# Kernel optimization log

Measured on AMD Instinct MI355X. Metric: run time of the kernel, lower is better.

## Reference

```python
import jax, jax.numpy as jnp
import numpy as np

B, S, D = 8, 1024, 768
H, HD = 12, 64  # heads, head dim (H*HD == D)
EPS = 1e-12


def setup_inputs() -> dict:
    key = jax.random.key(0)
    ks = jax.random.split(key, 8)
    s = 0.02
    return {
        "hidden_states": jax.random.normal(ks[0], (B, S, D), jnp.float32),
        "attention_mask": jnp.zeros((B, 1, 1, S), jnp.float32),
        "head_mask": jnp.ones((H,), jnp.float32),
        "Wq": jax.random.normal(ks[1], (D, H * HD), jnp.float32) * s,
        "bq": jnp.zeros((H * HD,), jnp.float32),
        "Wk": jax.random.normal(ks[2], (D, H * HD), jnp.float32) * s,
        "bk": jnp.zeros((H * HD,), jnp.float32),
        "Wv": jax.random.normal(ks[3], (D, H * HD), jnp.float32) * s,
        "bv": jnp.zeros((H * HD,), jnp.float32),
        "Wo": jax.random.normal(ks[4], (D, H * HD), jnp.float32) * s,  # torch Linear weight [out=D, in=H*HD]
        "bo": jnp.zeros((D,), jnp.float32),
        "gamma": jnp.ones((D,), jnp.float32),
        "beta": jnp.zeros((D,), jnp.float32),
    }


def reference(hidden_states, attention_mask, head_mask, Wq, bq, Wk, bk, Wv, bv, Wo, bo, gamma, beta):
    def heads(x):  # [B,S,H*HD] -> [B,H,S,HD]
        return x.reshape(B, S, H, HD).transpose(0, 2, 1, 3)

    q = heads(hidden_states @ Wq.T + bq)
    k = heads(hidden_states @ Wk.T + bk)
    v = heads(hidden_states @ Wv.T + bv)

    scores = jnp.einsum("bhqd,bhkd->bhqk", q, k) / np.sqrt(HD).astype(np.float32)
    scores = scores + attention_mask
    probs = jax.nn.softmax(scores, axis=-1)  # dropout p=0 (eval)
    ctx = jnp.einsum("bhqk,bhkd->bhqd", probs, v)  # [B,H,S,HD]

    # masked per-head output projection: Wo.T.view(H, HD, D)
    Wph = Wo.T.reshape(H, HD, D)
    proj = jnp.einsum("bhsd,hde,h->bse", ctx, Wph, head_mask) + bo

    # residual + LayerNorm
    x = proj + hidden_states
    mu = jnp.mean(x, axis=-1, keepdims=True)
    var = jnp.mean(jnp.square(x - mu), axis=-1, keepdims=True)
    out = (x - mu) * jax.lax.rsqrt(var + EPS) * gamma + beta
    return out
```

## Files before the change

### kernel.cpp

```cpp
#include <hip/hip_runtime.h>
#include <hip/hip_bf16.h>
#include <math.h>

#define Bn 8
#define Sn 1024
#define Dn 768
#define Hn 12
#define MROWS (Bn * Sn)

typedef __attribute__((ext_vector_type(8))) short short8;
typedef __attribute__((ext_vector_type(4))) float floatx4;

__device__ __forceinline__ unsigned short f2b(float x) {
    union { float f; unsigned u; } v; v.f = x;
    unsigned r = v.u + 0x7fffu + ((v.u >> 16) & 1u);
    return (unsigned short)(r >> 16);
}

__device__ __forceinline__ void gload16(const void* g, void* l) {
    __builtin_amdgcn_global_load_lds(
        (const __attribute__((address_space(1))) void*)g,
        (__attribute__((address_space(3))) void*)l, 16, 0, 0);
}

__global__ __launch_bounds__(256) void convert_all(const float* __restrict__ X,
                                                   const float* __restrict__ Wq, const float* __restrict__ Wk,
                                                   const float* __restrict__ Wv, const float* __restrict__ Wo,
                                                   unsigned short* __restrict__ Xb,
                                                   unsigned short* __restrict__ Wqb, unsigned short* __restrict__ Wkb,
                                                   unsigned short* __restrict__ Wvb, unsigned short* __restrict__ Wob) {
    const int id = blockIdx.x;
    const float* src;
    unsigned short* dst;
    int i;
    if (id < 6144) {
        src = X; dst = Xb;
        i = id * 256 + threadIdx.x;
    } else {
        const int y = (id - 6144) / 576;
        src = (y == 0) ? Wq : (y == 1) ? Wk : (y == 2) ? Wv : Wo;
        dst = (y == 0) ? Wqb : (y == 1) ? Wkb : (y == 2) ? Wvb : Wob;
        i = ((id - 6144) % 576) * 256 + threadIdx.x;
    }
    float4 v = reinterpret_cast<const float4*>(src)[i];
    ushort4 o;
    o.x = f2b(v.x); o.y = f2b(v.y); o.z = f2b(v.z); o.w = f2b(v.w);
    reinterpret_cast<ushort4*>(dst)[i] = o;
}

__global__ __launch_bounds__(256) void gemm_qkv(const unsigned short* __restrict__ A,
                                                const unsigned short* __restrict__ Wq,
                                                const unsigned short* __restrict__ Wk,
                                                const unsigned short* __restrict__ Wv,
                                                const float* __restrict__ bq,
                                                const float* __restrict__ bk,
                                                const float* __restrict__ bv,
                                                unsigned short* __restrict__ Qh,
                                                unsigned short* __restrict__ Kh,
                                                unsigned short* __restrict__ Vt) {
    __shared__ __align__(16) unsigned short As[128 * 64];
    __shared__ __align__(16) unsigned short Ws[128 * 64];
    const int id = blockIdx.x;
    const int by = id & 63;
    const int bx = id >> 6;
    const int mat = bx / 6;
    const int m0 = by * 128;
    const int n0 = (bx % 6) * 128;
    const unsigned short* W = (mat == 0) ? Wq : (mat == 1) ? Wk : Wv;
    const float* bias = (mat == 0) ? bq : (mat == 1) ? bk : bv;
    unsigned short* Cout = (mat == 0) ? Qh : (mat == 1) ? Kh : Vt;

    const int tid = threadIdx.x;
    const int w = tid >> 6, l = tid & 63, quad = l >> 4, mr = l & 15;
    const int wm = (w >> 1) * 64, wn = (w & 1) * 64;

    const unsigned short* gAsrc[4];
    const unsigned short* gWsrc[4];
    unsigned short* lAdst[4];
    unsigned short* lWdst[4];
#pragma unroll
    for (int j = 0; j < 4; j++) {
        const int u = tid + j * 256;
        const int r = u >> 3, c = u & 7;
        const int kq = (c ^ (r & 7)) * 8;
        gAsrc[j] = &A[(size_t)(m0 + r) * Dn + kq];
        gWsrc[j] = &W[(size_t)(n0 + r) * Dn + kq];
        lAdst[j] = &As[u * 8];
        lWdst[j] = &Ws[u * 8];
    }

    int aoff[4][2], woff[4][2];
#pragma unroll
    for (int i = 0; i < 4; i++) {
        const int ra = wm + i * 16 + mr;
        const int rw = wn + i * 16 + mr;
#pragma unroll
        for (int ks = 0; ks < 2; ks++) {
            aoff[i][ks] = (ra * 8 + ((quad + ks * 4) ^ (ra & 7))) * 8;
            woff[i][ks] = (rw * 8 + ((quad + ks * 4) ^ (rw & 7))) * 8;
        }
    }

    floatx4 acc[4][4];
#pragma unroll
    for (int i = 0; i < 4; i++)
#pragma unroll
        for (int j = 0; j < 4; j++) {
            floatx4 z = {0.f, 0.f, 0.f, 0.f};
            acc[i][j] = z;
        }

    for (int kt = 0; kt < 12; kt++) {
        const int k0 = kt * 64;
        __syncthreads();
#pragma unroll
        for (int j = 0; j < 4; j++) {
            gload16(gAsrc[j] + k0, lAdst[j]);
            gload16(gWsrc[j] + k0, lWdst[j]);
        }
        __syncthreads();

        short8 af[4][2], bf[4][2];
#pragma unroll
        for (int i = 0; i < 4; i++)
#pragma unroll
            for (int ks = 0; ks < 2; ks++) {
                af[i][ks] = *(const short8*)&As[aoff[i][ks]];
                bf[i][ks] = *(const short8*)&Ws[woff[i][ks]];
            }
#pragma unroll
        for (int ks = 0; ks < 2; ks++)
#pragma unroll
            for (int i = 0; i < 4; i++)
#pragma unroll
                for (int j = 0; j < 4; j++)
                    acc[i][j] = __builtin_amdgcn_mfma_f32_16x16x32_bf16(af[i][ks], bf[j][ks], acc[i][j], 0, 0, 0);
    }

#pragma unroll
    for (int j = 0; j < 4; j++) {
        const int col = n0 + wn + j * 16 + mr;
        const float bval = bias[col];
        const int h = col >> 6, d = col & 63;
#pragma unroll
        for (int i = 0; i < 4; i++) {
#pragma unroll
            for (int r = 0; r < 4; r++) {
                const int m = m0 + wm + i * 16 + quad * 4 + r;
                const float val = acc[i][j][r] + bval;
                const int b = m >> 10, s = m & 1023;
                const size_t base = (size_t)(b * Hn + h) << 16;
                if (mat == 2)
                    Cout[base + (size_t)d * 1024 + s] = f2b(val);
                else
                    Cout[base + (size_t)s * 64 + d] = f2b(val);
            }
        }
    }
}

__global__ __launch_bounds__(256) void gemm_out(const unsigned short* __restrict__ A,
                                                const unsigned short* __restrict__ W,
                                                const float* __restrict__ bias,
                                                const float* __restrict__ X,
                                                float* __restrict__ xres) {
    __shared__ __align__(16) unsigned short As[64 * 64];
    __shared__ __align__(16) unsigned short Ws[128 * 64];
    const int id = blockIdx.x;
    const int by = id & 127;
    const int bx = id >> 7;
    const int m0 = by * 64;
    const int n0 = bx * 128;

    const int tid = threadIdx.x;
    const int w = tid >> 6, l = tid & 63, quad = l >> 4, mr = l & 15;

    const unsigned short* gAsrc[2];
    unsigned short* lAdst[2];
#pragma unroll
    for (int j = 0; j < 2; j++) {
        const int u = tid + j * 256;
        const int r = u >> 3, c = u & 7;
        gAsrc[j] = &A[(size_t)(m0 + r) * Dn + (c ^ (r & 7)) * 8];
        lAdst[j] = &As[u * 8];
    }
    const unsigned short* gWsrc[4];
    unsigned short* lWdst[4];
#pragma unroll
    for (int j = 0; j < 4; j++) {
        const int u = tid + j * 256;
        const int r = u >> 3, c = u & 7;
        gWsrc[j] = &W[(size_t)(n0 + r) * Dn + (c ^ (r & 7)) * 8];
        lWdst[j] = &Ws[u * 8];
    }

    int aoff[4][2], woff[2][2];
#pragma unroll
    for (int i = 0; i < 4; i++) {
        const int ra = i * 16 + mr;
#pragma unroll
        for (int ks = 0; ks < 2; ks++)
            aoff[i][ks] = (ra * 8 + ((quad + ks * 4) ^ (ra & 7))) * 8;
    }
#pragma unroll
    for (int j = 0; j < 2; j++) {
        const int rw = w * 32 + j * 16 + mr;
#pragma unroll
        for (int ks = 0; ks < 2; ks++)
            woff[j][ks] = (rw * 8 + ((quad + ks * 4) ^ (rw & 7))) * 8;
    }

    floatx4 acc[4][2];
#pragma unroll
    for (int i = 0; i < 4; i++)
#pragma unroll
        for (int j = 0; j < 2; j++) {
            floatx4 z = {0.f, 0.f, 0.f, 0.f};
            acc[i][j] = z;
        }

    for (int kt = 0; kt < 12; kt++) {
        const int k0 = kt * 64;
        __syncthreads();
#pragma unroll
        for (int j = 0; j < 2; j++) gload16(gAsrc[j] + k0, lAdst[j]);
#pragma unroll
        for (int j = 0; j < 4; j++) gload16(gWsrc[j] + k0, lWdst[j]);
        __syncthreads();

        short8 af[4][2], bf[2][2];
#pragma unroll
        for (int i = 0; i < 4; i++)
#pragma unroll
            for (int ks = 0; ks < 2; ks++)
                af[i][ks] = *(const short8*)&As[aoff[i][ks]];
#pragma unroll
        for (int j = 0; j < 2; j++)
#pragma unroll
            for (int ks = 0; ks < 2; ks++)
                bf[j][ks] = *(const short8*)&Ws[woff[j][ks]];
#pragma unroll
        for (int ks = 0; ks < 2; ks++)
#pragma unroll
            for (int i = 0; i < 4; i++)
#pragma unroll
                for (int j = 0; j < 2; j++)
                    acc[i][j] = __builtin_amdgcn_mfma_f32_16x16x32_bf16(af[i][ks], bf[j][ks], acc[i][j], 0, 0, 0);
    }

#pragma unroll
    for (int j = 0; j < 2; j++) {
        const int col = n0 + w * 32 + j * 16 + mr;
        const float bval = bias[col];
#pragma unroll
        for (int i = 0; i < 4; i++) {
#pragma unroll
            for (int r = 0; r < 4; r++) {
                const int m = m0 + i * 16 + quad * 4 + r;
                xres[(size_t)m * Dn + col] = acc[i][j][r] + bval + X[(size_t)m * Dn + col];
            }
        }
    }
}

__global__ __launch_bounds__(256) void flash_attn_mfma(const unsigned short* __restrict__ Qh,
                                                       const unsigned short* __restrict__ Kh,
                                                       const unsigned short* __restrict__ Vt,
                                                       const float* __restrict__ mask,
                                                       const float* __restrict__ head_mask,
                                                       unsigned short* __restrict__ ctx) {
    __shared__ __align__(16) unsigned short Ks[64 * 72];
    __shared__ __align__(16) unsigned short Vs[64 * 72];
    __shared__ __align__(16) unsigned short Ps[128 * 72];
    __shared__ float msk[64];

    const int id = blockIdx.x;
    const int bh = id % 96;
    const int qt = id / 96;
    const int b = bh / Hn, h = bh % Hn;
    const int q0 = qt * 128;
    const int tid = threadIdx.x;
    const int w = tid >> 6, l = tid & 63, quad = l >> 4, mr = l & 15;
    const size_t hb = (size_t)(b * Hn + h) << 16;

    short8 aq[2][2];
#pragma unroll
    for (int i = 0; i < 2; i++)
#pragma unroll
        for (int ks = 0; ks < 2; ks++)
            aq[i][ks] = *(const short8*)&Qh[hb + (size_t)(q0 + w * 32 + i * 16 + mr) * 64 + ks * 32 + quad * 8];

    float l_s[2][4];
    floatx4 oacc[2][4];
#pragma unroll
    for (int i = 0; i < 2; i++) {
#pragma unroll
        for (int r = 0; r < 4; r++) l_s[i][r] = 0.f;
#pragma unroll
        for (int jj = 0; jj < 4; jj++) {
            floatx4 z = {0.f, 0.f, 0.f, 0.f};
            oacc[i][jj] = z;
        }
    }

    const int srow = tid >> 2;
    const int scol = (tid & 3) * 16;

    short8 pk0 = *(const short8*)&Kh[hb + (size_t)srow * 64 + scol];
    short8 pk1 = *(const short8*)&Kh[hb + (size_t)srow * 64 + scol + 8];
    short8 pv0 = *(const short8*)&Vt[hb + (size_t)srow * 1024 + scol];
    short8 pv1 = *(const short8*)&Vt[hb + (size_t)srow * 1024 + scol + 8];
    float pm = mask[b * Sn + (tid & 63)];

    for (int kt = 0; kt < Sn / 64; kt++) {
        __syncthreads();
        *(short8*)&Ks[srow * 72 + scol] = pk0;
        *(short8*)&Ks[srow * 72 + scol + 8] = pk1;
        *(short8*)&Vs[srow * 72 + scol] = pv0;
        *(short8*)&Vs[srow * 72 + scol + 8] = pv1;
        if (tid < 64) msk[tid] = pm;
        if (kt < Sn / 64 - 1) {
            const int k0 = (kt + 1) * 64;
            pk0 = *(const short8*)&Kh[hb + (size_t)(k0 + srow) * 64 + scol];
            pk1 = *(const short8*)&Kh[hb + (size_t)(k0 + srow) * 64 + scol + 8];
            pv0 = *(const short8*)&Vt[hb + (size_t)srow * 1024 + k0 + scol];
            pv1 = *(const short8*)&Vt[hb + (size_t)srow * 1024 + k0 + scol + 8];
            pm = mask[b * Sn + k0 + (tid & 63)];
        }
        __syncthreads();

        floatx4 sacc[2][4];
#pragma unroll
        for (int i = 0; i < 2; i++)
#pragma unroll
            for (int j = 0; j < 4; j++) {
                floatx4 z = {0.f, 0.f, 0.f, 0.f};
                sacc[i][j] = z;
            }
#pragma unroll
        for (int ks = 0; ks < 2; ks++) {
#pragma unroll
            for (int j = 0; j < 4; j++) {
                short8 bk = *(const short8*)&Ks[(j * 16 + mr) * 72 + ks * 32 + quad * 8];
                sacc[0][j] = __builtin_amdgcn_mfma_f32_16x16x32_bf16(aq[0][ks], bk, sacc[0][j], 0, 0, 0);
                sacc[1][j] = __builtin_amdgcn_mfma_f32_16x16x32_bf16(aq[1][ks], bk, sacc[1][j], 0, 0, 0);
            }
        }

#pragma unroll
        for (int i = 0; i < 2; i++) {
#pragma unroll
            for (int j = 0; j < 4; j++) {
                const float mk = msk[j * 16 + mr];
#pragma unroll
                for (int r = 0; r < 4; r++) {
                    const float p = __expf(sacc[i][j][r] * 0.125f + mk);
                    l_s[i][r] += p;
                    Ps[(w * 32 + i * 16 + quad * 4 + r) * 72 + j * 16 + mr] = f2b(p);
                }
            }
        }

#pragma unroll
        for (int ks = 0; ks < 2; ks++) {
            short8 ap0 = *(const short8*)&Ps[(w * 32 + mr) * 72 + ks * 32 + quad * 8];
            short8 ap1 = *(const short8*)&Ps[(w * 32 + 16 + mr) * 72 + ks * 32 + quad * 8];
#pragma unroll
            for (int jj = 0; jj < 4; jj++) {
                short8 bv = *(const short8*)&Vs[(jj * 16 + mr) * 72 + ks * 32 + quad * 8];
                oacc[0][jj] = __builtin_amdgcn_mfma_f32_16x16x32_bf16(ap0, bv, oacc[0][jj], 0, 0, 0);
                oacc[1][jj] = __builtin_amdgcn_mfma_f32_16x16x32_bf16(ap1, bv, oacc[1][jj], 0, 0, 0);
            }
        }
    }

    const float hm = head_mask[h];
    float inv[2][4];
#pragma unroll
    for (int i = 0; i < 2; i++)
#pragma unroll
        for (int r = 0; r < 4; r++) {
            float t = l_s[i][r];
            t += __shfl_xor(t, 1);
            t += __shfl_xor(t, 2);
            t += __shfl_xor(t, 4);
            t += __shfl_xor(t, 8);
            inv[i][r] = hm / t;
        }
#pragma unroll
    for (int i = 0; i < 2; i++)
#pragma unroll
        for (int jj = 0; jj < 4; jj++)
#pragma unroll
            for (int r = 0; r < 4; r++) {
                const int qrow = q0 + w * 32 + i * 16 + quad * 4 + r;
                ctx[(size_t)(b * Sn + qrow) * Dn + h * 64 + jj * 16 + mr] = f2b(oacc[i][jj][r] * inv[i][r]);
            }
}

__global__ __launch_bounds__(256) void ln_kernel(const float* __restrict__ x,
                                                 const float* __restrict__ gamma,
                                                 const float* __restrict__ beta,
                                                 float* __restrict__ out) {
    __shared__ float r1[4];
    __shared__ float r2[4];
    const int m = blockIdx.x;
    const int tid = threadIdx.x;
    const int w = tid >> 6, lane = tid & 63;

    float xv[3];
    float s = 0.f, ss = 0.f;
#pragma unroll
    for (int i = 0; i < 3; i++) {
        int j = tid + i * 256;
        float t = x[(size_t)m * Dn + j];
        xv[i] = t;
        s += t;
        ss += t * t;
    }
#pragma unroll
    for (int o = 1; o < 64; o <<= 1) {
        s += __shfl_xor(s, o);
        ss += __shfl_xor(ss, o);
    }
    if (lane == 0) { r1[w] = s; r2[w] = ss; }
    __syncthreads();
    const float sum = r1[0] + r1[1] + r1[2] + r1[3];
    const float sqs = r2[0] + r2[1] + r2[2] + r2[3];
    const float mu = sum * (1.0f / Dn);
    const float var = sqs * (1.0f / Dn) - mu * mu;
    const float rstd = rsqrtf(var + 1e-12f);
#pragma unroll
    for (int i = 0; i < 3; i++) {
        int j = tid + i * 256;
        out[(size_t)m * Dn + j] = (xv[i] - mu) * rstd * gamma[j] + beta[j];
    }
}

extern "C" void kernel_launch(void* const* d_in, const int* in_sizes, int n_in,
                              void* d_out, int out_size, void* d_ws, size_t ws_size,
                              hipStream_t stream) {
    const float* X         = (const float*)d_in[0];
    const float* mask      = (const float*)d_in[1];
    const float* head_mask = (const float*)d_in[2];
    const float* Wq        = (const float*)d_in[3];
    const float* bq        = (const float*)d_in[4];
    const float* Wk        = (const float*)d_in[5];
    const float* bk        = (const float*)d_in[6];
    const float* Wv        = (const float*)d_in[7];
    const float* bv        = (const float*)d_in[8];
    const float* Wo        = (const float*)d_in[9];
    const float* bo        = (const float*)d_in[10];
    const float* gamma     = (const float*)d_in[11];
    const float* beta      = (const float*)d_in[12];
    float* out = (float*)d_out;

    const size_t NE = (size_t)Bn * Sn * Dn;
    const size_t NW = (size_t)Dn * Dn;

    char* p = (char*)d_ws;
    unsigned short* Xb  = (unsigned short*)p;  p += NE * 2;
    unsigned short* Wqb = (unsigned short*)p;  p += NW * 2;
    unsigned short* Wkb = (unsigned short*)p;  p += NW * 2;
    unsigned short* Wvb = (unsigned short*)p;  p += NW * 2;
    unsigned short* Wob = (unsigned short*)p;  p += NW * 2;
    unsigned short* Qh  = (unsigned short*)p;  p += NE * 2;
    unsigned short* Kh  = (unsigned short*)p;  p += NE * 2;
    unsigned short* Vtb = (unsigned short*)p;  p += NE * 2;
    unsigned short* ctx = (unsigned short*)p;  p += NE * 2;
    float* xres = (float*)p;

    convert_all<<<8448, 256, 0, stream>>>(X, Wq, Wk, Wv, Wo, Xb, Wqb, Wkb, Wvb, Wob);

    gemm_qkv<<<1152, 256, 0, stream>>>(Xb, Wqb, Wkb, Wvb, bq, bk, bv, Qh, Kh, Vtb);

    flash_attn_mfma<<<768, 256, 0, stream>>>(Qh, Kh, Vtb, mask, head_mask, ctx);

    gemm_out<<<768, 256, 0, stream>>>(ctx, Wob, bo, X, xres);

    ln_kernel<<<MROWS, 256, 0, stream>>>(xres, gamma, beta, out);
}
```

Baseline: 224.9 us.

## Double-buffer LDS tiles in QKV and output GEMMs, vectorize V-transpose stores

Both projection GEMMs now keep two LDS buffers, so the next K-tile's global-to-LDS loads are issued before computing on the current tile. This hides global load latency and halves the barriers per K step. The QKV epilogue also writes the transposed V output as packed 4-element stores instead of scalar ones. The cost is doubled LDS use per block, which may lower occupancy.

```diff
diff --git a/kernel.cpp b/kernel.cpp
--- a/kernel.cpp
+++ b/kernel.cpp
@@ -48,6 +48,21 @@
     reinterpret_cast<ushort4*>(dst)[i] = o;
 }
 
+#define QKV_COMPUTE(Ab, Wb)                                                    \
+    {                                                                          \
+        short8 af[4][2], bf[4][2];                                             \
+        _Pragma("unroll") for (int i = 0; i < 4; i++)                          \
+            _Pragma("unroll") for (int ks = 0; ks < 2; ks++) {                 \
+                af[i][ks] = *(const short8*)&(Ab)[aoff[i][ks]];                \
+                bf[i][ks] = *(const short8*)&(Wb)[woff[i][ks]];                \
+            }                                                                  \
+        _Pragma("unroll") for (int ks = 0; ks < 2; ks++)                       \
+            _Pragma("unroll") for (int i = 0; i < 4; i++)                      \
+                _Pragma("unroll") for (int j = 0; j < 4; j++)                  \
+                    acc[i][j] = __builtin_amdgcn_mfma_f32_16x16x32_bf16(       \
+                        af[i][ks], bf[j][ks], acc[i][j], 0, 0, 0);             \
+    }
+
 __global__ __launch_bounds__(256) void gemm_qkv(const unsigned short* __restrict__ A,
                                                 const unsigned short* __restrict__ Wq,
                                                 const unsigned short* __restrict__ Wk,
@@ -58,8 +73,8 @@
                                                 unsigned short* __restrict__ Qh,
                                                 unsigned short* __restrict__ Kh,
                                                 unsigned short* __restrict__ Vt) {
-    __shared__ __align__(16) unsigned short As[128 * 64];
-    __shared__ __align__(16) unsigned short Ws[128 * 64];
+    __shared__ __align__(16) unsigned short As[2][128 * 64];
+    __shared__ __align__(16) unsigned short Ws[2][128 * 64];
     const int id = blockIdx.x;
     const int by = id & 63;
     const int bx = id >> 6;
@@ -85,8 +100,8 @@
         const int kq = (c ^ (r & 7)) * 8;
         gAsrc[j] = &A[(size_t)(m0 + r) * Dn + kq];
         gWsrc[j] = &W[(size_t)(n0 + r) * Dn + kq];
-        lAdst[j] = &As[u * 8];
-        lWdst[j] = &Ws[u * 8];
+        lAdst[j] = &As[0][u * 8];
+        lWdst[j] = &Ws[0][u * 8];
     }
 
     int aoff[4][2], woff[4][2];
@@ -110,31 +125,38 @@
             acc[i][j] = z;
         }
 
-    for (int kt = 0; kt < 12; kt++) {
-        const int k0 = kt * 64;
+    const unsigned short* Af = &As[0][0];
+    const unsigned short* Wf = &Ws[0][0];
+
+#pragma unroll
+    for (int j = 0; j < 4; j++) {
+        gload16(gAsrc[j], lAdst[j]);
+        gload16(gWsrc[j], lWdst[j]);
+    }
+    __syncthreads();
+
+    for (int kt = 0; kt < 12; kt += 2) {
+        {
+            const int k0 = (kt + 1) * 64;
+#pragma unroll
+            for (int j = 0; j < 4; j++) {
+                gload16(gAsrc[j] + k0, lAdst[j] + 8192);
+                gload16(gWsrc[j] + k0, lWdst[j] + 8192);
+            }
+        }
+        QKV_COMPUTE(Af, Wf);
         __syncthreads();
-#pragma unroll
-        for (int j = 0; j < 4; j++) {
-            gload16(gAsrc[j] + k0, lAdst[j]);
-            gload16(gWsrc[j] + k0, lWdst[j]);
-        }
+
+        if (kt + 2 < 12) {
+            const int k0 = (kt + 2) * 64;
+#pragma unroll
+            for (int j = 0; j < 4; j++) {
+                gload16(gAsrc[j] + k0, lAdst[j]);
+                gload16(gWsrc[j] + k0, lWdst[j]);
+            }
+        }
+        QKV_COMPUTE(Af + 8192, Wf + 8192);
         __syncthreads();
-
-        short8 af[4][2], bf[4][2];
-#pragma unroll
-        for (int i = 0; i < 4; i++)
-#pragma unroll
-            for (int ks = 0; ks < 2; ks++) {
-                af[i][ks] = *(const short8*)&As[aoff[i][ks]];
-                bf[i][ks] = *(const short8*)&Ws[woff[i][ks]];
-            }
-#pragma unroll
-        for (int ks = 0; ks < 2; ks++)
-#pragma unroll
-            for (int i = 0; i < 4; i++)
-#pragma unroll
-                for (int j = 0; j < 4; j++)
-                    acc[i][j] = __builtin_amdgcn_mfma_f32_16x16x32_bf16(af[i][ks], bf[j][ks], acc[i][j], 0, 0, 0);
     }
 
 #pragma unroll
@@ -144,28 +166,50 @@
         const int h = col >> 6, d = col & 63;
 #pragma unroll
         for (int i = 0; i < 4; i++) {
-#pragma unroll
-            for (int r = 0; r < 4; r++) {
-                const int m = m0 + wm + i * 16 + quad * 4 + r;
-                const float val = acc[i][j][r] + bval;
-                const int b = m >> 10, s = m & 1023;
-                const size_t base = (size_t)(b * Hn + h) << 16;
-                if (mat == 2)
-                    Cout[base + (size_t)d * 1024 + s] = f2b(val);
-                else
-                    Cout[base + (size_t)s * 64 + d] = f2b(val);
-            }
-        }
-    }
-}
+            const int mbase = m0 + wm + i * 16 + quad * 4;
+            const int b = mbase >> 10, s0 = mbase & 1023;
+            const size_t base = (size_t)(b * Hn + h) << 16;
+            if (mat == 2) {
+                ushort4 o;
+                o.x = f2b(acc[i][j][0] + bval);
+                o.y = f2b(acc[i][j][1] + bval);
+                o.z = f2b(acc[i][j][2] + bval);
+                o.w = f2b(acc[i][j][3] + bval);
+                *reinterpret_cast<ushort4*>(&Cout[base + (size_t)d * 1024 + s0]) = o;
+            } else {
+#pragma unroll
+                for (int r = 0; r < 4; r++) {
+                    const float val = acc[i][j][r] + bval;
+                    Cout[base + (size_t)(s0 + r) * 64 + d] = f2b(val);
+                }
+            }
+        }
+    }
+}
+
+#define OUT_COMPUTE(Ab, Wb)                                                    \
+    {                                                                          \
+        short8 af[4][2], bf[2][2];                                             \
+        _Pragma("unroll") for (int i = 0; i < 4; i++)                          \
+            _Pragma("unroll") for (int ks = 0; ks < 2; ks++)                   \
+                af[i][ks] = *(const short8*)&(Ab)[aoff[i][ks]];                \
+        _Pragma("unroll") for (int j = 0; j < 2; j++)                          \
+            _Pragma("unroll") for (int ks = 0; ks < 2; ks++)                   \
+                bf[j][ks] = *(const short8*)&(Wb)[woff[j][ks]];                \
+        _Pragma("unroll") for (int ks = 0; ks < 2; ks++)                       \
+            _Pragma("unroll") for (int i = 0; i < 4; i++)                      \
+                _Pragma("unroll") for (int j = 0; j < 2; j++)                  \
+                    acc[i][j] = __builtin_amdgcn_mfma_f32_16x16x32_bf16(       \
+                        af[i][ks], bf[j][ks], acc[i][j], 0, 0, 0);             \
+    }
 
 __global__ __launch_bounds__(256) void gemm_out(const unsigned short* __restrict__ A,
                                                 const unsigned short* __restrict__ W,
                                                 const float* __restrict__ bias,
                                                 const float* __restrict__ X,
                                                 float* __restrict__ xres) {
-    __shared__ __align__(16) unsigned short As[64 * 64];
-    __shared__ __align__(16) unsigned short Ws[128 * 64];
+    __shared__ __align__(16) unsigned short As[2][64 * 64];
+    __shared__ __align__(16) unsigned short Ws[2][128 * 64];
     const int id = blockIdx.x;
     const int by = id & 127;
     const int bx = id >> 7;
@@ -182,7 +226,7 @@
         const int u = tid + j * 256;
         const int r = u >> 3, c = u & 7;
         gAsrc[j] = &A[(size_t)(m0 + r) * Dn + (c ^ (r & 7)) * 8];
-        lAdst[j] = &As[u * 8];
+        lAdst[j] = &As[0][u * 8];
     }
     const unsigned short* gWsrc[4];
     unsigned short* lWdst[4];
@@ -191,7 +235,7 @@
         const int u = tid + j * 256;
         const int r = u >> 3, c = u & 7;
         gWsrc[j] = &W[(size_t)(n0 + r) * Dn + (c ^ (r & 7)) * 8];
-        lWdst[j] = &Ws[u * 8];
+        lWdst[j] = &Ws[0][u * 8];
     }
 
     int aoff[4][2], woff[2][2];
@@ -219,33 +263,35 @@
             acc[i][j] = z;
         }
 
-    for (int kt = 0; kt < 12; kt++) {
-        const int k0 = kt * 64;
+    const unsigned short* Af = &As[0][0];
+    const unsigned short* Wf = &Ws[0][0];
+
+#pragma unroll
+    for (int j = 0; j < 2; j++) gload16(gAsrc[j], lAdst[j]);
+#pragma unroll
+    for (int j = 0; j < 4; j++) gload16(gWsrc[j], lWdst[j]);
+    __syncthreads();
+
+    for (int kt = 0; kt < 12; kt += 2) {
+        {
+            const int k0 = (kt + 1) * 64;
+#pragma unroll
+            for (int j = 0; j < 2; j++) gload16(gAsrc[j] + k0, lAdst[j] + 4096);
+#pragma unroll
+            for (int j = 0; j < 4; j++) gload16(gWsrc[j] + k0, lWdst[j] + 8192);
+        }
+        OUT_COMPUTE(Af, Wf);
         __syncthreads();
-#pragma unroll
-        for (int j = 0; j < 2; j++) gload16(gAsrc[j] + k0, lAdst[j]);
-#pragma unroll
-        for (int j = 0; j < 4; j++) gload16(gWsrc[j] + k0, lWdst[j]);
+
+        if (kt + 2 < 12) {
+            const int k0 = (kt + 2) * 64;
+#pragma unroll
+            for (int j = 0; j < 2; j++) gload16(gAsrc[j] + k0, lAdst[j]);
+#pragma unroll
+            for (int j = 0; j < 4; j++) gload16(gWsrc[j] + k0, lWdst[j]);
+        }
+        OUT_COMPUTE(Af + 4096, Wf + 8192);
         __syncthreads();
-
-        short8 af[4][2], bf[2][2];
-#pragma unroll
-        for (int i = 0; i < 4; i++)
-#pragma unroll
-            for (int ks = 0; ks < 2; ks++)
-                af[i][ks] = *(const short8*)&As[aoff[i][ks]];
-#pragma unroll
-        for (int j = 0; j < 2; j++)
-#pragma unroll
-            for (int ks = 0; ks < 2; ks++)
-                bf[j][ks] = *(const short8*)&Ws[woff[j][ks]];
-#pragma unroll
-        for (int ks = 0; ks < 2; ks++)
-#pragma unroll
-            for (int i = 0; i < 4; i++)
-#pragma unroll
-                for (int j = 0; j < 2; j++)
-                    acc[i][j] = __builtin_amdgcn_mfma_f32_16x16x32_bf16(af[i][ks], bf[j][ks], acc[i][j], 0, 0, 0);
     }
 
 #pragma unroll
```

Measured after the change: 223.8 us. Within noise of the previous version (-0.5%).
